# Kernel optimization log

Measured on AMD Instinct MI355X. Metric: run time of the kernel, lower is better.

The kernel has to match this reference:

```python
import jax, jax.numpy as jnp
import numpy as np

N, K, F, E = 50000, 32, 128, 8

def setup_inputs() -> dict:
    key = jax.random.key(0)
    k1, k2, k3, k4, k5 = jax.random.split(key, 5)
    nodes = jax.random.normal(k1, (N, F), dtype=jnp.float32)
    nlist = jax.random.randint(k2, (N, K), 0, N, dtype=jnp.int64)
    edges = jax.random.normal(k3, (N, K, E), dtype=jnp.float32)
    inv_degree = jax.random.uniform(k4, (N,), dtype=jnp.float32)
    w = jax.random.normal(k5, (F, F, E), dtype=jnp.float32)
    return {"nodes": nodes, "nlist": nlist, "edges": edges,
            "inv_degree": inv_degree, "w": w}

def reference(nodes, nlist, edges, inv_degree, w):
    # gather neighbor features: [N, K, F]
    sliced = nodes[nlist]
    # 3-way contraction with neighbor-sum and inverse-degree scaling
    # edges: ijn (N,K,E); sliced: ijl (N,K,F); w: lmn (F,F,E); inv_degree: i
    out = jnp.einsum('ijn,ijl,lmn,i->im', edges, sliced, w, inv_degree)
    # activation is None (linear) per init_kwargs
    return out
```

## Files before the change

### kernel.cpp

```cpp
#include <hip/hip_runtime.h>
#include <hip/hip_bf16.h>

static constexpr int NN  = 50000;
static constexpr int KNB = 32;
static constexpr int F   = 128;
static constexpr int E   = 8;
static constexpr int TI  = 16;
static constexpr int LN  = F * E;

typedef __attribute__((ext_vector_type(8))) short short8v;
typedef __attribute__((ext_vector_type(4))) float f32x4;

__device__ __forceinline__ unsigned short f2bf(float x) {
    unsigned u = __float_as_uint(x);
    unsigned r = (u + 0x7fff + ((u >> 16) & 1)) >> 16;
    return (unsigned short)r;
}

__global__ void prep_w_kernel(const float* __restrict__ w, unsigned short* __restrict__ w2f) {
    int o  = blockIdx.x * 256 + threadIdx.x;
    int e8 = o & 7, kq = (o >> 3) & 3, m = (o >> 5) & 127, kb = o >> 12;
    int k  = kb * 32 + kq * 4 + (e8 & 3) + ((e8 >> 2) << 4);
    int l  = k >> 3, n = k & 7;
    w2f[o] = f2bf(w[(size_t)(l * F + m) * E + n]);
}

__global__ void prep_nodes_kernel(const float* __restrict__ nodes, unsigned short* __restrict__ nb) {
    int t = blockIdx.x * 256 + threadIdx.x;
    const float4* s = (const float4*)nodes + (size_t)t * 2;
    float4 a = s[0], b = s[1];
    uint4 pk;
    pk.x = (unsigned)f2bf(a.x) | ((unsigned)f2bf(a.y) << 16);
    pk.y = (unsigned)f2bf(a.z) | ((unsigned)f2bf(a.w) << 16);
    pk.z = (unsigned)f2bf(b.x) | ((unsigned)f2bf(b.y) << 16);
    pk.w = (unsigned)f2bf(b.z) | ((unsigned)f2bf(b.w) << 16);
    ((uint4*)nb)[t] = pk;
}

template<bool NB>
__global__ __launch_bounds__(512, 8)
void mp_main_kernel(const float* __restrict__ nodes,
                    const unsigned short* __restrict__ nodesBf,
                    const int*   __restrict__ nlist,
                    const float* __restrict__ edges,
                    const float* __restrict__ inv_degree,
                    const unsigned short* __restrict__ w2f,
                    float* __restrict__ out)
{
    __shared__ unsigned short tS[TI * LN];
    const int tid    = threadIdx.x;
    const int wv     = __builtin_amdgcn_readfirstlane(tid >> 6);
    const int lane   = tid & 63;
    const int i_base = blockIdx.x * TI;
    char* tB = (char*)tS;

    for (int it = 0; it < 2; ++it) {
        const int row = wv * 2 + it;
        const int i   = i_base + row;
        const int*   nl = nlist + (size_t)i * KNB;
        const float* ep = edges + (size_t)i * (KNB * E);

        float2 p0[4], p1[4];
        #pragma unroll
        for (int q = 0; q < 4; ++q) { p0[q] = make_float2(0.f, 0.f); p1[q] = make_float2(0.f, 0.f); }

        #pragma unroll
        for (int j = 0; j < KNB; ++j) {
            unsigned idx = (unsigned)nl[j];
            if (idx >= (unsigned)NN) idx = 0u;
            idx = __builtin_amdgcn_readfirstlane(idx);
            unsigned g;
            if (NB) {
                g = ((const unsigned*)(nodesBf + (size_t)idx * F))[lane];
            } else {
                const float2 fv = ((const float2*)(nodes + (size_t)idx * F))[lane];
                g = ((unsigned)f2bf(fv.y) << 16) | (unsigned)f2bf(fv.x);
            }
            const float2 e01 = *(const float2*)(ep + j * 8 + 0);
            const float2 e23 = *(const float2*)(ep + j * 8 + 2);
            const float2 e45 = *(const float2*)(ep + j * 8 + 4);
            const float2 e67 = *(const float2*)(ep + j * 8 + 6);
            float2 vv0, vv1;
            vv0.x = __uint_as_float(g << 16);         vv0.y = vv0.x;
            vv1.x = __uint_as_float(g & 0xffff0000u); vv1.y = vv1.x;
            asm("v_pk_fma_f32 %0, %1, %2, %0" : "+v"(p0[0]) : "s"(e01), "v"(vv0));
            asm("v_pk_fma_f32 %0, %1, %2, %0" : "+v"(p0[1]) : "s"(e23), "v"(vv0));
            asm("v_pk_fma_f32 %0, %1, %2, %0" : "+v"(p0[2]) : "s"(e45), "v"(vv0));
            asm("v_pk_fma_f32 %0, %1, %2, %0" : "+v"(p0[3]) : "s"(e67), "v"(vv0));
            asm("v_pk_fma_f32 %0, %1, %2, %0" : "+v"(p1[0]) : "s"(e01), "v"(vv1));
            asm("v_pk_fma_f32 %0, %1, %2, %0" : "+v"(p1[1]) : "s"(e23), "v"(vv1));
            asm("v_pk_fma_f32 %0, %1, %2, %0" : "+v"(p1[2]) : "s"(e45), "v"(vv1));
            asm("v_pk_fma_f32 %0, %1, %2, %0" : "+v"(p1[3]) : "s"(e67), "v"(vv1));
        }

        uint4 pk0, pk1;
        asm("v_cvt_pk_bf16_f32 %0, %1, %2" : "=v"(pk0.x) : "v"(p0[0].x), "v"(p0[0].y));
        asm("v_cvt_pk_bf16_f32 %0, %1, %2" : "=v"(pk0.y) : "v"(p0[1].x), "v"(p0[1].y));
        asm("v_cvt_pk_bf16_f32 %0, %1, %2" : "=v"(pk0.z) : "v"(p0[2].x), "v"(p0[2].y));
        asm("v_cvt_pk_bf16_f32 %0, %1, %2" : "=v"(pk0.w) : "v"(p0[3].x), "v"(p0[3].y));
        asm("v_cvt_pk_bf16_f32 %0, %1, %2" : "=v"(pk1.x) : "v"(p1[0].x), "v"(p1[0].y));
        asm("v_cvt_pk_bf16_f32 %0, %1, %2" : "=v"(pk1.y) : "v"(p1[1].x), "v"(p1[1].y));
        asm("v_cvt_pk_bf16_f32 %0, %1, %2" : "=v"(pk1.z) : "v"(p1[2].x), "v"(p1[2].y));
        asm("v_cvt_pk_bf16_f32 %0, %1, %2" : "=v"(pk1.w) : "v"(p1[3].x), "v"(p1[3].y));

        const int p2 = (lane >> 2) & 1;
        const int s  = (row & 7) << 4;
        const int rb = row * (LN * 2);
        const uint4 first  = p2 ? pk1 : pk0;
        const uint4 second = p2 ? pk0 : pk1;
        *(uint4*)(tB + rb + ((lane * 32 + (p2 << 4))      ^ s)) = first;
        *(uint4*)(tB + rb + ((lane * 32 + 16 - (p2 << 4)) ^ s)) = second;
    }
    __syncthreads();

    const int colm = lane & 15;
    const int kq   = lane >> 4;
    const int mt   = wv;

    f32x4 c0 = {0.f, 0.f, 0.f, 0.f};

    const int arow = colm * (LN * 2);
    const int asw  = (colm & 7) << 4;

    #pragma unroll 4
    for (int kb = 0; kb < LN / 32; ++kb) {
        union { short8v v; uint2 u[2]; } af;
        af.u[0] = *(const uint2*)(tB + arow + ((kb * 64      + kq * 8) ^ asw));
        af.u[1] = *(const uint2*)(tB + arow + ((kb * 64 + 32 + kq * 8) ^ asw));
        union { short8v v; uint4 u; } b0;
        b0.u = *(const uint4*)(w2f + ((size_t)((kb * 128 + mt * 16 + colm) * 4 + kq)) * 8);
        c0 = __builtin_amdgcn_mfma_f32_16x16x32_bf16(af.v, b0.v, c0, 0, 0, 0);
    }

    #pragma unroll
    for (int r = 0; r < 4; ++r) {
        const int ii = kq * 4 + r;
        const int gi = i_base + ii;
        out[(size_t)gi * F + mt * 16 + colm] = inv_degree[gi] * c0[r];
    }
}

__global__ __launch_bounds__(256, 2)
void mp_fused_fallback(const float* __restrict__ nodes, const int* __restrict__ nlist,
                       const float* __restrict__ edges, const float* __restrict__ inv_degree,
                       const float* __restrict__ w, float* __restrict__ out)
{
    __shared__ float tLds[TI * F * E];
    const int tid = threadIdx.x;
    const int i_base = blockIdx.x * TI;
    {
        const int l = tid & (F - 1);
        const int half = __builtin_amdgcn_readfirstlane(tid >> 7);
        for (int g = 0; g < TI / 2; ++g) {
            const int ii = g * 2 + half;
            const int i = i_base + ii;
            float acc[E];
            #pragma unroll
            for (int n = 0; n < E; ++n) acc[n] = 0.f;
            const int* nl = nlist + i * KNB;
            const float* ep = edges + (size_t)i * (KNB * E);
            #pragma unroll 4
            for (int j = 0; j < KNB; ++j) {
                unsigned idx = (unsigned)nl[j];
                if (idx >= (unsigned)NN) idx = 0u;
                const float v = nodes[idx * F + l];
                #pragma unroll
                for (int n = 0; n < E; ++n) acc[n] = __builtin_fmaf(ep[j * E + n], v, acc[n]);
            }
            float4* dst = (float4*)&tLds[ii * (F * E) + l * E];
            dst[0] = make_float4(acc[0], acc[1], acc[2], acc[3]);
            dst[1] = make_float4(acc[4], acc[5], acc[6], acc[7]);
        }
    }
    __syncthreads();
    const int m_lo = tid & 63;
    const int q = __builtin_amdgcn_readfirstlane(tid >> 6);
    float accA[TI], accB[TI];
    #pragma unroll
    for (int ii = 0; ii < TI; ++ii) { accA[ii] = 0.f; accB[ii] = 0.f; }
    for (int lq = 0; lq < F / 4; ++lq) {
        const int l = q * (F / 4) + lq;
        const float4* wp0 = (const float4*)&w[(size_t)l * (F * E) + (size_t)m_lo * E];
        const float4* wp1 = (const float4*)&w[(size_t)l * (F * E) + (size_t)(m_lo + 64) * E];
        const float4 w0a = wp0[0], w0b = wp0[1];
        const float4 w1a = wp1[0], w1b = wp1[1];
        #pragma unroll
        for (int ii = 0; ii < TI; ++ii) {
            const float4* tp = (const float4*)&tLds[ii * (F * E) + l * E];
            const float4 ta = tp[0], tb = tp[1];
            float sA = accA[ii], sB = accB[ii];
            sA = __builtin_fmaf(ta.x, w0a.x, sA); sA = __builtin_fmaf(ta.y, w0a.y, sA);
            sA = __builtin_fmaf(ta.z, w0a.z, sA); sA = __builtin_fmaf(ta.w, w0a.w, sA);
            sA = __builtin_fmaf(tb.x, w0b.x, sA); sA = __builtin_fmaf(tb.y, w0b.y, sA);
            sA = __builtin_fmaf(tb.z, w0b.z, sA); sA = __builtin_fmaf(tb.w, w0b.w, sA);
            sB = __builtin_fmaf(ta.x, w1a.x, sB); sB = __builtin_fmaf(ta.y, w1a.y, sB);
            sB = __builtin_fmaf(ta.z, w1a.z, sB); sB = __builtin_fmaf(ta.w, w1a.w, sB);
            sB = __builtin_fmaf(tb.x, w1b.x, sB); sB = __builtin_fmaf(tb.y, w1b.y, sB);
            sB = __builtin_fmaf(tb.z, w1b.z, sB); sB = __builtin_fmaf(tb.w, w1b.w, sB);
            accA[ii] = sA; accB[ii] = sB;
        }
    }
    __syncthreads();
    float* pLds = tLds;
    #pragma unroll
    for (int ii = 0; ii < TI; ++ii) {
        pLds[q * (TI * F) + ii * F + m_lo] = accA[ii];
        pLds[q * (TI * F) + ii * F + m_lo + 64] = accB[ii];
    }
    __syncthreads();
    #pragma unroll
    for (int r = 0; r < (TI * F) / 256; ++r) {
        const int o = r * 256 + tid;
        const int ii = o >> 7;
        const int m = o & (F - 1);
        const float s = pLds[0 * (TI * F) + ii * F + m] + pLds[1 * (TI * F) + ii * F + m]
                      + pLds[2 * (TI * F) + ii * F + m] + pLds[3 * (TI * F) + ii * F + m];
        const int i = i_base + ii;
        out[(size_t)i * F + m] = inv_degree[i] * s;
    }
}

extern "C" void kernel_launch(void* const* d_in, const int* in_sizes, int n_in,
                              void* d_out, int out_size, void* d_ws, size_t ws_size,
                              hipStream_t stream) {
    const float* nodes      = (const float*)d_in[0];
    const int*   nlist      = (const int*)d_in[1];
    const float* edges      = (const float*)d_in[2];
    const float* inv_degree = (const float*)d_in[3];
    const float* w          = (const float*)d_in[4];
    float* out = (float*)d_out;
    (void)in_sizes; (void)n_in; (void)out_size;

    const size_t need_w2 = (size_t)LN * F * 2;
    const size_t need_nb = (size_t)NN * F * 2;

    if (ws_size < need_w2) {
        mp_fused_fallback<<<dim3(NN / TI), dim3(256), 0, stream>>>(
            nodes, nlist, edges, inv_degree, w, out);
        return;
    }
    unsigned short* w2f = (unsigned short*)d_ws;
    unsigned short* nb  = (unsigned short*)((char*)d_ws + need_w2);

    prep_w_kernel<<<dim3((LN * F) / 256), dim3(256), 0, stream>>>(w, w2f);
    if (ws_size >= need_w2 + need_nb) {
        prep_nodes_kernel<<<dim3(NN * F / 8 / 256), dim3(256), 0, stream>>>(nodes, nb);
        mp_main_kernel<true><<<dim3(NN / TI), dim3(512), 0, stream>>>(
            nodes, nb, nlist, edges, inv_degree, w2f, out);
    } else {
        mp_main_kernel<false><<<dim3(NN / TI), dim3(512), 0, stream>>>(
            nodes, nb, nlist, edges, inv_degree, w2f, out);
    }
}
```

Baseline: 101.3 us.

## Stage edges in LDS and process two node rows per wave with wider gathers

The block's edge tile is copied into shared memory up front, so the per-row edge weights are read from LDS instead of as scalar global loads. Each wave now handles its two rows at once, 32 lanes per row, and each lane gathers 4 bf16 features (uint2) with plain FMAs instead of inline packed FMA. The LDS swizzle is reworked to match the new write pattern, and the non-bf16 template path is removed so the fallback is used when workspace is short. The cost is extra LDS (16 KB per block) and a lower occupancy hint (6 instead of 8).

```diff
diff --git a/kernel.cpp b/kernel.cpp
--- a/kernel.cpp
+++ b/kernel.cpp
@@ -37,10 +37,8 @@
     ((uint4*)nb)[t] = pk;
 }
 
-template<bool NB>
-__global__ __launch_bounds__(512, 8)
-void mp_main_kernel(const float* __restrict__ nodes,
-                    const unsigned short* __restrict__ nodesBf,
+__global__ __launch_bounds__(512, 6)
+void mp_main_kernel(const unsigned short* __restrict__ nodesBf,
                     const int*   __restrict__ nlist,
                     const float* __restrict__ edges,
                     const float* __restrict__ inv_degree,
@@ -48,68 +46,75 @@
                     float* __restrict__ out)
 {
     __shared__ unsigned short tS[TI * LN];
+    __shared__ float eS[TI * KNB * E];
     const int tid    = threadIdx.x;
     const int wv     = __builtin_amdgcn_readfirstlane(tid >> 6);
     const int lane   = tid & 63;
+    const int h      = lane >> 5;
+    const int c      = lane & 31;
     const int i_base = blockIdx.x * TI;
     char* tB = (char*)tS;
 
-    for (int it = 0; it < 2; ++it) {
-        const int row = wv * 2 + it;
-        const int i   = i_base + row;
-        const int*   nl = nlist + (size_t)i * KNB;
-        const float* ep = edges + (size_t)i * (KNB * E);
-
-        float2 p0[4], p1[4];
-        #pragma unroll
-        for (int q = 0; q < 4; ++q) { p0[q] = make_float2(0.f, 0.f); p1[q] = make_float2(0.f, 0.f); }
+    {
+        const float4* src = (const float4*)(edges + (size_t)i_base * (KNB * E));
+        float4* dst = (float4*)eS;
+        #pragma unroll
+        for (int r = 0; r < 8; ++r) dst[r * 512 + tid] = src[r * 512 + tid];
+    }
+    __syncthreads();
+
+    {
+        const int row = wv * 2 + h;
+        const int* nlA = nlist + (size_t)(i_base + wv * 2) * KNB;
+        const int* nlB = nlA + KNB;
+
+        float acc[4][8];
+        #pragma unroll
+        for (int k = 0; k < 4; ++k)
+            #pragma unroll
+            for (int n = 0; n < 8; ++n) acc[k][n] = 0.f;
+
+        const unsigned cb = (unsigned)c * 8u;
+        const float2* ep = (const float2*)(eS + row * (KNB * E));
 
         #pragma unroll
         for (int j = 0; j < KNB; ++j) {
-            unsigned idx = (unsigned)nl[j];
-            if (idx >= (unsigned)NN) idx = 0u;
-            idx = __builtin_amdgcn_readfirstlane(idx);
-            unsigned g;
-            if (NB) {
-                g = ((const unsigned*)(nodesBf + (size_t)idx * F))[lane];
-            } else {
-                const float2 fv = ((const float2*)(nodes + (size_t)idx * F))[lane];
-                g = ((unsigned)f2bf(fv.y) << 16) | (unsigned)f2bf(fv.x);
+            unsigned iA = (unsigned)nlA[j]; if (iA >= (unsigned)NN) iA = 0u;
+            unsigned iB = (unsigned)nlB[j]; if (iB >= (unsigned)NN) iB = 0u;
+            const unsigned voff = (h ? iB : iA) * 256u + cb;
+            const uint2 g = *(const uint2*)((const char*)nodesBf + voff);
+            const float2 e01 = ep[j * 4 + 0];
+            const float2 e23 = ep[j * 4 + 1];
+            const float2 e45 = ep[j * 4 + 2];
+            const float2 e67 = ep[j * 4 + 3];
+            const float vk[4] = { __uint_as_float(g.x << 16),
+                                  __uint_as_float(g.x & 0xffff0000u),
+                                  __uint_as_float(g.y << 16),
+                                  __uint_as_float(g.y & 0xffff0000u) };
+            #pragma unroll
+            for (int k = 0; k < 4; ++k) {
+                acc[k][0] = __builtin_fmaf(e01.x, vk[k], acc[k][0]);
+                acc[k][1] = __builtin_fmaf(e01.y, vk[k], acc[k][1]);
+                acc[k][2] = __builtin_fmaf(e23.x, vk[k], acc[k][2]);
+                acc[k][3] = __builtin_fmaf(e23.y, vk[k], acc[k][3]);
+                acc[k][4] = __builtin_fmaf(e45.x, vk[k], acc[k][4]);
+                acc[k][5] = __builtin_fmaf(e45.y, vk[k], acc[k][5]);
+                acc[k][6] = __builtin_fmaf(e67.x, vk[k], acc[k][6]);
+                acc[k][7] = __builtin_fmaf(e67.y, vk[k], acc[k][7]);
             }
-            const float2 e01 = *(const float2*)(ep + j * 8 + 0);
-            const float2 e23 = *(const float2*)(ep + j * 8 + 2);
-            const float2 e45 = *(const float2*)(ep + j * 8 + 4);
-            const float2 e67 = *(const float2*)(ep + j * 8 + 6);
-            float2 vv0, vv1;
-            vv0.x = __uint_as_float(g << 16);         vv0.y = vv0.x;
-            vv1.x = __uint_as_float(g & 0xffff0000u); vv1.y = vv1.x;
-            asm("v_pk_fma_f32 %0, %1, %2, %0" : "+v"(p0[0]) : "s"(e01), "v"(vv0));
-            asm("v_pk_fma_f32 %0, %1, %2, %0" : "+v"(p0[1]) : "s"(e23), "v"(vv0));
-            asm("v_pk_fma_f32 %0, %1, %2, %0" : "+v"(p0[2]) : "s"(e45), "v"(vv0));
-            asm("v_pk_fma_f32 %0, %1, %2, %0" : "+v"(p0[3]) : "s"(e67), "v"(vv0));
-            asm("v_pk_fma_f32 %0, %1, %2, %0" : "+v"(p1[0]) : "s"(e01), "v"(vv1));
-            asm("v_pk_fma_f32 %0, %1, %2, %0" : "+v"(p1[1]) : "s"(e23), "v"(vv1));
-            asm("v_pk_fma_f32 %0, %1, %2, %0" : "+v"(p1[2]) : "s"(e45), "v"(vv1));
-            asm("v_pk_fma_f32 %0, %1, %2, %0" : "+v"(p1[3]) : "s"(e67), "v"(vv1));
-        }
-
-        uint4 pk0, pk1;
-        asm("v_cvt_pk_bf16_f32 %0, %1, %2" : "=v"(pk0.x) : "v"(p0[0].x), "v"(p0[0].y));
-        asm("v_cvt_pk_bf16_f32 %0, %1, %2" : "=v"(pk0.y) : "v"(p0[1].x), "v"(p0[1].y));
-        asm("v_cvt_pk_bf16_f32 %0, %1, %2" : "=v"(pk0.z) : "v"(p0[2].x), "v"(p0[2].y));
-        asm("v_cvt_pk_bf16_f32 %0, %1, %2" : "=v"(pk0.w) : "v"(p0[3].x), "v"(p0[3].y));
-        asm("v_cvt_pk_bf16_f32 %0, %1, %2" : "=v"(pk1.x) : "v"(p1[0].x), "v"(p1[0].y));
-        asm("v_cvt_pk_bf16_f32 %0, %1, %2" : "=v"(pk1.y) : "v"(p1[1].x), "v"(p1[1].y));
-        asm("v_cvt_pk_bf16_f32 %0, %1, %2" : "=v"(pk1.z) : "v"(p1[2].x), "v"(p1[2].y));
-        asm("v_cvt_pk_bf16_f32 %0, %1, %2" : "=v"(pk1.w) : "v"(p1[3].x), "v"(p1[3].y));
-
-        const int p2 = (lane >> 2) & 1;
-        const int s  = (row & 7) << 4;
+        }
+
+        const int sw = ((row & 7) << 4) ^ ((c & 7) << 4);
         const int rb = row * (LN * 2);
-        const uint4 first  = p2 ? pk1 : pk0;
-        const uint4 second = p2 ? pk0 : pk1;
-        *(uint4*)(tB + rb + ((lane * 32 + (p2 << 4))      ^ s)) = first;
-        *(uint4*)(tB + rb + ((lane * 32 + 16 - (p2 << 4)) ^ s)) = second;
+        #pragma unroll
+        for (int t = 0; t < 4; ++t) {
+            uint4 pk;
+            asm("v_cvt_pk_bf16_f32 %0, %1, %2" : "=v"(pk.x) : "v"(acc[t][0]), "v"(acc[t][1]));
+            asm("v_cvt_pk_bf16_f32 %0, %1, %2" : "=v"(pk.y) : "v"(acc[t][2]), "v"(acc[t][3]));
+            asm("v_cvt_pk_bf16_f32 %0, %1, %2" : "=v"(pk.z) : "v"(acc[t][4]), "v"(acc[t][5]));
+            asm("v_cvt_pk_bf16_f32 %0, %1, %2" : "=v"(pk.w) : "v"(acc[t][6]), "v"(acc[t][7]));
+            *(uint4*)(tB + rb + ((((c * 4 + t) * 16)) ^ sw)) = pk;
+        }
     }
     __syncthreads();
 
@@ -124,9 +129,10 @@
 
     #pragma unroll 4
     for (int kb = 0; kb < LN / 32; ++kb) {
+        const int lx = (kb & 7) << 4;
         union { short8v v; uint2 u[2]; } af;
-        af.u[0] = *(const uint2*)(tB + arow + ((kb * 64      + kq * 8) ^ asw));
-        af.u[1] = *(const uint2*)(tB + arow + ((kb * 64 + 32 + kq * 8) ^ asw));
+        af.u[0] = *(const uint2*)(tB + arow + ((kb * 64      + kq * 8) ^ asw ^ lx));
+        af.u[1] = *(const uint2*)(tB + arow + ((kb * 64 + 32 + kq * 8) ^ asw ^ lx));
         union { short8v v; uint4 u; } b0;
         b0.u = *(const uint4*)(w2f + ((size_t)((kb * 128 + mt * 16 + colm) * 4 + kq)) * 8);
         c0 = __builtin_amdgcn_mfma_f32_16x16x32_bf16(af.v, b0.v, c0, 0, 0, 0);
@@ -234,7 +240,7 @@
     const size_t need_w2 = (size_t)LN * F * 2;
     const size_t need_nb = (size_t)NN * F * 2;
 
-    if (ws_size < need_w2) {
+    if (ws_size < need_w2 + need_nb) {
         mp_fused_fallback<<<dim3(NN / TI), dim3(256), 0, stream>>>(
             nodes, nlist, edges, inv_degree, w, out);
         return;
@@ -243,12 +249,7 @@
     unsigned short* nb  = (unsigned short*)((char*)d_ws + need_w2);
 
     prep_w_kernel<<<dim3((LN * F) / 256), dim3(256), 0, stream>>>(w, w2f);
-    if (ws_size >= need_w2 + need_nb) {
-        prep_nodes_kernel<<<dim3(NN * F / 8 / 256), dim3(256), 0, stream>>>(nodes, nb);
-        mp_main_kernel<true><<<dim3(NN / TI), dim3(512), 0, stream>>>(
-            nodes, nb, nlist, edges, inv_degree, w2f, out);
-    } else {
-        mp_main_kernel<false><<<dim3(NN / TI), dim3(512), 0, stream>>>(
-            nodes, nb, nlist, edges, inv_degree, w2f, out);
-    }
-}
+    prep_nodes_kernel<<<dim3(NN * F / 8 / 256), dim3(256), 0, stream>>>(nodes, nb);
+    mp_main_kernel<<<dim3(NN / TI), dim3(512), 0, stream>>>(
+        nb, nlist, edges, inv_degree, w2f, out);
+}
```

Measured after the change: 116.8 us. 15.3% more time.

## Software-pipeline neighbor gathers with batched inline-asm loads and manual vmcnt waits

Applied to the files above, without the earlier changes.

The gather loop now issues neighbor-row loads in batches of eight using inline global_load_dword with precomputed offsets, keeping up to 24 loads in flight and waiting with explicit s_waitcnt before consuming each batch. This hides gather latency instead of relying on compiler scheduling per neighbor. Packed FMAs become scalar fmaf with float4 edge loads, the fp32-node path is dropped (small workspaces take the fallback kernel), and the launch-bounds occupancy hint drops from 8 to 6 to make room for the extra registers. The risks are lower occupancy and the correctness of the hand-written waitcnt around compiler-scheduled code.

```diff
diff --git a/kernel.cpp b/kernel.cpp
--- a/kernel.cpp
+++ b/kernel.cpp
@@ -16,6 +16,8 @@
     unsigned r = (u + 0x7fff + ((u >> 16) & 1)) >> 16;
     return (unsigned short)r;
 }
+__device__ __forceinline__ float bf2f_lo(unsigned g) { return __uint_as_float(g << 16); }
+__device__ __forceinline__ float bf2f_hi(unsigned g) { return __uint_as_float(g & 0xffff0000u); }
 
 __global__ void prep_w_kernel(const float* __restrict__ w, unsigned short* __restrict__ w2f) {
     int o  = blockIdx.x * 256 + threadIdx.x;
@@ -37,10 +39,57 @@
     ((uint4*)nb)[t] = pk;
 }
 
-template<bool NB>
-__global__ __launch_bounds__(512, 8)
-void mp_main_kernel(const float* __restrict__ nodes,
-                    const unsigned short* __restrict__ nodesBf,
+#define ISSUE8(B)                                                          \
+    asm volatile(                                                          \
+        "global_load_dword %0, %8, %16\n\t"                                \
+        "global_load_dword %1, %9, %16\n\t"                                \
+        "global_load_dword %2, %10, %16\n\t"                               \
+        "global_load_dword %3, %11, %16\n\t"                               \
+        "global_load_dword %4, %12, %16\n\t"                               \
+        "global_load_dword %5, %13, %16\n\t"                               \
+        "global_load_dword %6, %14, %16\n\t"                               \
+        "global_load_dword %7, %15, %16"                                   \
+        : "=&v"(g[(B)+0]), "=&v"(g[(B)+1]), "=&v"(g[(B)+2]), "=&v"(g[(B)+3]), \
+          "=&v"(g[(B)+4]), "=&v"(g[(B)+5]), "=&v"(g[(B)+6]), "=&v"(g[(B)+7])  \
+        : "v"(vo[0]), "v"(vo[1]), "v"(vo[2]), "v"(vo[3]),                  \
+          "v"(vo[4]), "v"(vo[5]), "v"(vo[6]), "v"(vo[7]),                  \
+          "s"(nodesBf)                                                     \
+        : "memory")
+
+#define MKVO(B)                                                            \
+    _Pragma("unroll")                                                      \
+    for (int q = 0; q < 8; ++q) {                                          \
+        unsigned idx = (unsigned)nl[(B) + q];       \
+        if (idx >= (unsigned)NN) idx = 0u;                                 \
+        vo[q] = idx * 256u + lane4;                                        \
+    }
+
+#define WAIT8(NSTR, B)                                                     \
+    asm volatile("s_waitcnt vmcnt(" NSTR ")"                               \
+        : "+v"(g[(B)+0]), "+v"(g[(B)+1]), "+v"(g[(B)+2]), "+v"(g[(B)+3]),  \
+          "+v"(g[(B)+4]), "+v"(g[(B)+5]), "+v"(g[(B)+6]), "+v"(g[(B)+7])   \
+        :: "memory")
+
+#define CONSUME8(B)                                                        \
+    _Pragma("unroll")                                                      \
+    for (int q = 0; q < 8; ++q) {                                          \
+        const int j = (B) + q;                                             \
+        const float v0 = bf2f_lo(g[(B) + q]);                              \
+        const float v1 = bf2f_hi(g[(B) + q]);                              \
+        const float4 e0 = *(const float4*)(ep + j * 8);       \
+        const float4 e1 = *(const float4*)(ep + j * 8 + 4);                \
+        a0[0] = __builtin_fmaf(e0.x, v0, a0[0]); a1[0] = __builtin_fmaf(e0.x, v1, a1[0]); \
+        a0[1] = __builtin_fmaf(e0.y, v0, a0[1]); a1[1] = __builtin_fmaf(e0.y, v1, a1[1]); \
+        a0[2] = __builtin_fmaf(e0.z, v0, a0[2]); a1[2] = __builtin_fmaf(e0.z, v1, a1[2]); \
+        a0[3] = __builtin_fmaf(e0.w, v0, a0[3]); a1[3] = __builtin_fmaf(e0.w, v1, a1[3]); \
+        a0[4] = __builtin_fmaf(e1.x, v0, a0[4]); a1[4] = __builtin_fmaf(e1.x, v1, a1[4]); \
+        a0[5] = __builtin_fmaf(e1.y, v0, a0[5]); a1[5] = __builtin_fmaf(e1.y, v1, a1[5]); \
+        a0[6] = __builtin_fmaf(e1.z, v0, a0[6]); a1[6] = __builtin_fmaf(e1.z, v1, a1[6]); \
+        a0[7] = __builtin_fmaf(e1.w, v0, a0[7]); a1[7] = __builtin_fmaf(e1.w, v1, a1[7]); \
+    }
+
+__global__ __launch_bounds__(512, 6)
+void mp_main_kernel(const unsigned short* __restrict__ nodesBf,
                     const int*   __restrict__ nlist,
                     const float* __restrict__ edges,
                     const float* __restrict__ inv_degree,
@@ -53,6 +102,7 @@
     const int lane   = tid & 63;
     const int i_base = blockIdx.x * TI;
     char* tB = (char*)tS;
+    const unsigned lane4 = (unsigned)lane * 4u;
 
     for (int it = 0; it < 2; ++it) {
         const int row = wv * 2 + it;
@@ -60,49 +110,30 @@
         const int*   nl = nlist + (size_t)i * KNB;
         const float* ep = edges + (size_t)i * (KNB * E);
 
-        float2 p0[4], p1[4];
+        float a0[E], a1[E];
         #pragma unroll
-        for (int q = 0; q < 4; ++q) { p0[q] = make_float2(0.f, 0.f); p1[q] = make_float2(0.f, 0.f); }
-
-        #pragma unroll
-        for (int j = 0; j < KNB; ++j) {
-            unsigned idx = (unsigned)nl[j];
-            if (idx >= (unsigned)NN) idx = 0u;
-            idx = __builtin_amdgcn_readfirstlane(idx);
-            unsigned g;
-            if (NB) {
-                g = ((const unsigned*)(nodesBf + (size_t)idx * F))[lane];
-            } else {
-                const float2 fv = ((const float2*)(nodes + (size_t)idx * F))[lane];
-                g = ((unsigned)f2bf(fv.y) << 16) | (unsigned)f2bf(fv.x);
-            }
-            const float2 e01 = *(const float2*)(ep + j * 8 + 0);
-            const float2 e23 = *(const float2*)(ep + j * 8 + 2);
-            const float2 e45 = *(const float2*)(ep + j * 8 + 4);
-            const float2 e67 = *(const float2*)(ep + j * 8 + 6);
-            float2 vv0, vv1;
-            vv0.x = __uint_as_float(g << 16);         vv0.y = vv0.x;
-            vv1.x = __uint_as_float(g & 0xffff0000u); vv1.y = vv1.x;
-            asm("v_pk_fma_f32 %0, %1, %2, %0" : "+v"(p0[0]) : "s"(e01), "v"(vv0));
-            asm("v_pk_fma_f32 %0, %1, %2, %0" : "+v"(p0[1]) : "s"(e23), "v"(vv0));
-            asm("v_pk_fma_f32 %0, %1, %2, %0" : "+v"(p0[2]) : "s"(e45), "v"(vv0));
-            asm("v_pk_fma_f32 %0, %1, %2, %0" : "+v"(p0[3]) : "s"(e67), "v"(vv0));
-            asm("v_pk_fma_f32 %0, %1, %2, %0" : "+v"(p1[0]) : "s"(e01), "v"(vv1));
-            asm("v_pk_fma_f32 %0, %1, %2, %0" : "+v"(p1[1]) : "s"(e23), "v"(vv1));
-            asm("v_pk_fma_f32 %0, %1, %2, %0" : "+v"(p1[2]) : "s"(e45), "v"(vv1));
-            asm("v_pk_fma_f32 %0, %1, %2, %0" : "+v"(p1[3]) : "s"(e67), "v"(vv1));
-        }
+        for (int n = 0; n < E; ++n) { a0[n] = 0.f; a1[n] = 0.f; }
+
+        unsigned g[32];
+        unsigned vo[8];
+        MKVO(0);  ISSUE8(0);
+        MKVO(8);  ISSUE8(8);
+        MKVO(16); ISSUE8(16);
+        WAIT8("16", 0);  CONSUME8(0);
+        MKVO(24); ISSUE8(24);
+        WAIT8("16", 8);  CONSUME8(8);
+        WAIT8("8", 16);  CONSUME8(16);
+        WAIT8("0", 24);  CONSUME8(24);
 
         uint4 pk0, pk1;
-        asm("v_cvt_pk_bf16_f32 %0, %1, %2" : "=v"(pk0.x) : "v"(p0[0].x), "v"(p0[0].y));
-        asm("v_cvt_pk_bf16_f32 %0, %1, %2" : "=v"(pk0.y) : "v"(p0[1].x), "v"(p0[1].y));
-        asm("v_cvt_pk_bf16_f32 %0, %1, %2" : "=v"(pk0.z) : "v"(p0[2].x), "v"(p0[2].y));
-        asm("v_cvt_pk_bf16_f32 %0, %1, %2" : "=v"(pk0.w) : "v"(p0[3].x), "v"(p0[3].y));
-        asm("v_cvt_pk_bf16_f32 %0, %1, %2" : "=v"(pk1.x) : "v"(p1[0].x), "v"(p1[0].y));
-        asm("v_cvt_pk_bf16_f32 %0, %1, %2" : "=v"(pk1.y) : "v"(p1[1].x), "v"(p1[1].y));
-        asm("v_cvt_pk_bf16_f32 %0, %1, %2" : "=v"(pk1.z) : "v"(p1[2].x), "v"(p1[2].y));
-        asm("v_cvt_pk_bf16_f32 %0, %1, %2" : "=v"(pk1.w) : "v"(p1[3].x), "v"(p1[3].y));
-
+        asm("v_cvt_pk_bf16_f32 %0, %1, %2" : "=v"(pk0.x) : "v"(a0[0]), "v"(a0[1]));
+        asm("v_cvt_pk_bf16_f32 %0, %1, %2" : "=v"(pk0.y) : "v"(a0[2]), "v"(a0[3]));
+        asm("v_cvt_pk_bf16_f32 %0, %1, %2" : "=v"(pk0.z) : "v"(a0[4]), "v"(a0[5]));
+        asm("v_cvt_pk_bf16_f32 %0, %1, %2" : "=v"(pk0.w) : "v"(a0[6]), "v"(a0[7]));
+        asm("v_cvt_pk_bf16_f32 %0, %1, %2" : "=v"(pk1.x) : "v"(a1[0]), "v"(a1[1]));
+        asm("v_cvt_pk_bf16_f32 %0, %1, %2" : "=v"(pk1.y) : "v"(a1[2]), "v"(a1[3]));
+        asm("v_cvt_pk_bf16_f32 %0, %1, %2" : "=v"(pk1.z) : "v"(a1[4]), "v"(a1[5]));
+        asm("v_cvt_pk_bf16_f32 %0, %1, %2" : "=v"(pk1.w) : "v"(a1[6]), "v"(a1[7]));
         const int p2 = (lane >> 2) & 1;
         const int s  = (row & 7) << 4;
         const int rb = row * (LN * 2);
@@ -234,7 +265,7 @@
     const size_t need_w2 = (size_t)LN * F * 2;
     const size_t need_nb = (size_t)NN * F * 2;
 
-    if (ws_size < need_w2) {
+    if (ws_size < need_w2 + need_nb) {
         mp_fused_fallback<<<dim3(NN / TI), dim3(256), 0, stream>>>(
             nodes, nlist, edges, inv_degree, w, out);
         return;
@@ -243,12 +274,7 @@
     unsigned short* nb  = (unsigned short*)((char*)d_ws + need_w2);
 
     prep_w_kernel<<<dim3((LN * F) / 256), dim3(256), 0, stream>>>(w, w2f);
-    if (ws_size >= need_w2 + need_nb) {
-        prep_nodes_kernel<<<dim3(NN * F / 8 / 256), dim3(256), 0, stream>>>(nodes, nb);
-        mp_main_kernel<true><<<dim3(NN / TI), dim3(512), 0, stream>>>(
-            nodes, nb, nlist, edges, inv_degree, w2f, out);
-    } else {
-        mp_main_kernel<false><<<dim3(NN / TI), dim3(512), 0, stream>>>(
-            nodes, nb, nlist, edges, inv_degree, w2f, out);
-    }
-}
+    prep_nodes_kernel<<<dim3(NN * F / 8 / 256), dim3(256), 0, stream>>>(nodes, nb);
+    mp_main_kernel<<<dim3(NN / TI), dim3(512), 0, stream>>>(
+        nb, nlist, edges, inv_degree, w2f, out);
+}
```

Measured after the change: 102.7 us. Within noise of the previous version (+1.4%).
